# Kernel tuning notes

Hardware: AMD Instinct MI355X
Metric: run time of the kernel (lower is better)

## Reference

```python
import jax, jax.numpy as jnp
import numpy as np

N_BODIES = 3
NDOF = 3 * N_BODIES          # 9
HIDDEN = 128                 # max(16, 256//2)
EPS2 = 0.1 ** 2              # softening_eps^2
MASS_EPS = 1e-8
B = 262144
# torch.triu_indices(3, 3, 1) -> pairs (0,1),(0,2),(1,2)
PAIR_I = jnp.array([0, 0, 1])
PAIR_J = jnp.array([1, 2, 2])


def setup_inputs() -> dict:
    key = jax.random.key(0)
    ks = jax.random.split(key, 7)
    inv = lambda n: 1.0 / np.sqrt(n)  # torch Linear default init scale (uniform bound)
    return {
        "z": jax.random.normal(ks[0], (B, 2 * NDOF), jnp.float32),
        "log_m_body": jnp.zeros((N_BODIES,), jnp.float32),
        "W1": jax.random.uniform(ks[1], (HIDDEN, 1), jnp.float32, -inv(1), inv(1)),
        "b1": jax.random.uniform(ks[2], (HIDDEN,), jnp.float32, -inv(1), inv(1)),
        "W2": jax.random.uniform(ks[3], (HIDDEN, HIDDEN), jnp.float32, -inv(HIDDEN), inv(HIDDEN)),
        "b2": jax.random.uniform(ks[4], (HIDDEN,), jnp.float32, -inv(HIDDEN), inv(HIDDEN)),
        "W3": jax.random.uniform(ks[5], (1, HIDDEN), jnp.float32, -inv(HIDDEN), inv(HIDDEN)),
        "b3": jax.random.uniform(ks[6], (1,), jnp.float32, -inv(HIDDEN), inv(HIDDEN)),
    }


def _hamiltonian(z, log_m_body, W1, b1, W2, b2, W3, b3):
    q, p = z[:, :NDOF], z[:, NDOF:]
    # kinetic: T(p) = 0.5 * sum p^2 / m  (tied per-body learned mass)
    minv = 1.0 / (jnp.repeat(jnp.exp(log_m_body), 3) + MASS_EPS)  # [ndof]
    T = 0.5 * jnp.sum(p * p * minv, axis=1)                        # [B]
    # potential: softened inverse pairwise distance -> tiny MLP -> sum over pairs
    qb = q.reshape(-1, N_BODIES, 3)
    diff = qb[:, PAIR_I] - qb[:, PAIR_J]                           # [B,3,3]
    d = jnp.sqrt(jnp.sum(diff * diff, axis=-1) + EPS2)             # [B,3]
    s = (1.0 / d)[..., None]                                       # [B,3,1]
    h = jax.nn.silu(s @ W1.T + b1)                                 # [B,3,128]
    h = jax.nn.silu(h @ W2.T + b2)                                 # [B,3,128]
    v = (h @ W3.T + b3)[..., 0]                                    # [B,3]
    V = jnp.sum(v, axis=1)                                         # [B]
    return T + V


def reference(z, log_m_body, W1, b1, W2, b2, W3, b3):
    # dz/dt = J grad_z H with canonical J: dq/dt = dH/dp, dp/dt = -dH/dq
    grad = jax.grad(
        lambda zz: jnp.sum(_hamiltonian(zz, log_m_body, W1, b1, W2, b2, W3, b3))
    )(z)
    dqdt = grad[:, NDOF:]
    dpdt = -grad[:, :NDOF]
    return jnp.concatenate([dqdt, dpdt], axis=1)
```

## Files before the change

kernel.cpp:

```cpp
#include <hip/hip_runtime.h>
#include <math.h>

#define HIDDEN       128
#define TABLE_N      2048
#define SMAX         10.0f
#define E            8
#define TB_THREADS   128
#define MAIN_THREADS 256
#define EPS2         0.01f
#define MASS_EPS     1e-8f
#define W2PAD        (HIDDEN + 1)

__global__ __launch_bounds__(TB_THREADS)
void build_table_kernel(const float* __restrict__ W1,
                        const float* __restrict__ b1,
                        const float* __restrict__ W2,
                        const float* __restrict__ b2,
                        const float* __restrict__ W3,
                        const float* __restrict__ logm,
                        float* __restrict__ table)
{
    const int tid = threadIdx.x;
    const int e0  = blockIdx.x * E;
    __shared__ float w2s[HIDDEN * W2PAD];
    __shared__ float sh[HIDDEN * E];

    {
        const float4* w2v = (const float4*)W2;
        #pragma unroll
        for (int k = 0; k < (HIDDEN * HIDDEN / 4) / TB_THREADS; ++k) {
            int idx = k * TB_THREADS + tid;
            float4 v = w2v[idx];
            int fi  = idx << 2;
            int row = fi >> 7;
            int col = fi & (HIDDEN - 1);
            float* dst = &w2s[row * W2PAD + col];
            dst[0] = v.x; dst[1] = v.y; dst[2] = v.z; dst[3] = v.w;
        }
    }

    if (blockIdx.x == 0 && tid < 3)
        table[TABLE_N + tid] = 1.0f / (expf(logm[tid]) + MASS_EPS);

    const float ds  = SMAX / (float)(TABLE_N - 1);
    const float w1  = W1[tid];
    const float bb1 = b1[tid];

    float sp1[E];
    #pragma unroll
    for (int e = 0; e < E; ++e) {
        float s  = (float)(e0 + e) * ds;
        float u1 = w1 * s + bb1;
        float sg = 1.0f / (1.0f + expf(-u1));
        sh[tid * E + e] = u1 * sg;
        sp1[e] = sg * (1.0f + u1 * (1.0f - sg));
    }
    __syncthreads();

    float u2[E];
    #pragma unroll
    for (int e = 0; e < E; ++e) u2[e] = b2[tid];
    for (int j = 0; j < HIDDEN; ++j) {
        float w = w2s[tid * W2PAD + j];
        #pragma unroll
        for (int e = 0; e < E; ++e) u2[e] += w * sh[j * E + e];
    }

    const float w3 = W3[tid];
    float a[E];
    #pragma unroll
    for (int e = 0; e < E; ++e) {
        float sg = 1.0f / (1.0f + expf(-u2[e]));
        a[e] = w3 * sg * (1.0f + u2[e] * (1.0f - sg));
    }
    __syncthreads();
    #pragma unroll
    for (int e = 0; e < E; ++e) sh[tid * E + e] = a[e];
    __syncthreads();

    float gv[E];
    #pragma unroll
    for (int e = 0; e < E; ++e) gv[e] = 0.0f;
    for (int i = 0; i < HIDDEN; ++i) {
        float w = w2s[i * W2PAD + tid];
        #pragma unroll
        for (int e = 0; e < E; ++e) gv[e] += w * sh[i * E + e];
    }
    __syncthreads();

    #pragma unroll
    for (int e = 0; e < E; ++e) sh[tid * E + e] = w1 * sp1[e] * gv[e];
    __syncthreads();
    if (tid < E) {
        float g = 0.0f;
        for (int j = 0; j < HIDDEN; ++j) g += sh[j * E + tid];
        table[e0 + tid] = g;
    }
}

__global__ __launch_bounds__(MAIN_THREADS)
void hnn_grad_kernel(const float4* __restrict__ z4,
                     const float* __restrict__ table,
                     float4* __restrict__ out4)
{
    __shared__ alignas(16) float buf[MAIN_THREADS * 18];
    float4* bufv = (float4*)buf;
    const int tid = threadIdx.x;
    const long long base4 = (long long)blockIdx.x * (MAIN_THREADS * 18 / 4);

    #pragma unroll
    for (int k = 0; k < 4; ++k)
        bufv[k * MAIN_THREADS + tid] = z4[base4 + k * MAIN_THREADS + tid];
    if (tid < MAIN_THREADS / 2)
        bufv[4 * MAIN_THREADS + tid] = z4[base4 + 4 * MAIN_THREADS + tid];
    __syncthreads();

    float q[9], p[9];
    #pragma unroll
    for (int c = 0; c < 9; ++c) q[c] = buf[tid * 18 + c];
    #pragma unroll
    for (int c = 0; c < 9; ++c) p[c] = buf[tid * 18 + 9 + c];

    const float minv0 = table[TABLE_N + 0];
    const float minv1 = table[TABLE_N + 1];
    const float minv2 = table[TABLE_N + 2];

    float dq[9], dp[9];
    #pragma unroll
    for (int c = 0; c < 3; ++c) {
        dq[c]     = p[c]     * minv0;
        dq[3 + c] = p[3 + c] * minv1;
        dq[6 + c] = p[6 + c] * minv2;
    }
    #pragma unroll
    for (int c = 0; c < 9; ++c) dp[c] = 0.0f;

    const float scale = (float)(TABLE_N - 1) / SMAX;
    const int pi[3] = {0, 0, 1};
    const int pj[3] = {1, 2, 2};
    #pragma unroll
    for (int k = 0; k < 3; ++k) {
        const int i = pi[k] * 3, j = pj[k] * 3;
        float dx = q[i]     - q[j];
        float dy = q[i + 1] - q[j + 1];
        float dz = q[i + 2] - q[j + 2];
        float r2 = dx * dx + dy * dy + dz * dz + EPS2;
        float s  = 1.0f / sqrtf(r2);
        float x  = s * scale;
        int  idx = (int)x;
        idx = idx > (TABLE_N - 2) ? (TABLE_N - 2) : idx;
        float f  = x - (float)idx;
        float t0 = table[idx], t1 = table[idx + 1];
        float g  = t0 + f * (t1 - t0);
        float w = g * s * s * s;
        dp[i]     += w * dx;  dp[i + 1] += w * dy;  dp[i + 2] += w * dz;
        dp[j]     -= w * dx;  dp[j + 1] -= w * dy;  dp[j + 2] -= w * dz;
    }

    __syncthreads();
    #pragma unroll
    for (int c = 0; c < 9; ++c) buf[tid * 18 + c]     = dq[c];
    #pragma unroll
    for (int c = 0; c < 9; ++c) buf[tid * 18 + 9 + c] = dp[c];
    __syncthreads();

    #pragma unroll
    for (int k = 0; k < 4; ++k)
        out4[base4 + k * MAIN_THREADS + tid] = bufv[k * MAIN_THREADS + tid];
    if (tid < MAIN_THREADS / 2)
        out4[base4 + 4 * MAIN_THREADS + tid] = bufv[4 * MAIN_THREADS + tid];
}

extern "C" void kernel_launch(void* const* d_in, const int* in_sizes, int n_in,
                              void* d_out, int out_size, void* d_ws, size_t ws_size,
                              hipStream_t stream)
{
    const float* z   = (const float*)d_in[0];
    const float* lm  = (const float*)d_in[1];
    const float* W1  = (const float*)d_in[2];
    const float* b1  = (const float*)d_in[3];
    const float* W2  = (const float*)d_in[4];
    const float* b2  = (const float*)d_in[5];
    const float* W3  = (const float*)d_in[6];
    float* table = (float*)d_ws;

    hipLaunchKernelGGL(build_table_kernel, dim3(TABLE_N / E), dim3(TB_THREADS),
                       0, stream, W1, b1, W2, b2, W3, lm, table);

    const int B = in_sizes[0] / 18;
    hipLaunchKernelGGL(hnn_grad_kernel, dim3(B / MAIN_THREADS), dim3(MAIN_THREADS),
                       0, stream, (const float4*)z, table, (float4*)d_out);
}
```

Before: 97.45 us.

## Split table-build matvecs across two thread halves, stage table in LDS, nontemporal I/O

The table-build kernel now runs 256 threads, with each half computing partial sums over half of the hidden dimension and combining them through shared memory. Its final reduction over hidden units becomes a two-level tree. The main kernel copies the interpolation table into LDS before doing the random-index lookups, and uses nontemporal loads and stores for the streaming z and output traffic. Costs are extra shared memory, more barriers, and a per-block table copy that adds global reads.

```diff
diff --git a/kernel.cpp b/kernel.cpp
--- a/kernel.cpp
+++ b/kernel.cpp
@@ -5,11 +5,13 @@
 #define TABLE_N      2048
 #define SMAX         10.0f
 #define E            8
-#define TB_THREADS   128
+#define TB_THREADS   256
 #define MAIN_THREADS 256
 #define EPS2         0.01f
 #define MASS_EPS     1e-8f
 #define W2PAD        (HIDDEN + 1)
+
+typedef float vf4 __attribute__((ext_vector_type(4)));
 
 __global__ __launch_bounds__(TB_THREADS)
 void build_table_kernel(const float* __restrict__ W1,
@@ -20,17 +22,21 @@
                         const float* __restrict__ logm,
                         float* __restrict__ table)
 {
-    const int tid = threadIdx.x;
-    const int e0  = blockIdx.x * E;
+    const int tid  = threadIdx.x;
+    const int unit = tid & 127;
+    const int half = tid >> 7;
+    const int e0   = blockIdx.x * E;
+
     __shared__ float w2s[HIDDEN * W2PAD];
     __shared__ float sh[HIDDEN * E];
+    __shared__ float part[TB_THREADS * E];
 
     {
-        const float4* w2v = (const float4*)W2;
-        #pragma unroll
-        for (int k = 0; k < (HIDDEN * HIDDEN / 4) / TB_THREADS; ++k) {
+        const vf4* w2v = (const vf4*)W2;
+        #pragma unroll
+        for (int k = 0; k < 16; ++k) {
             int idx = k * TB_THREADS + tid;
-            float4 v = w2v[idx];
+            vf4 v = w2v[idx];
             int fi  = idx << 2;
             int row = fi >> 7;
             int col = fi & (HIDDEN - 1);
@@ -43,8 +49,8 @@
         table[TABLE_N + tid] = 1.0f / (expf(logm[tid]) + MASS_EPS);
 
     const float ds  = SMAX / (float)(TABLE_N - 1);
-    const float w1  = W1[tid];
-    const float bb1 = b1[tid];
+    const float w1  = W1[unit];
+    const float bb1 = b1[unit];
 
     float sp1[E];
     #pragma unroll
@@ -52,67 +58,99 @@
         float s  = (float)(e0 + e) * ds;
         float u1 = w1 * s + bb1;
         float sg = 1.0f / (1.0f + expf(-u1));
-        sh[tid * E + e] = u1 * sg;
+        if (half == 0) sh[unit * E + e] = u1 * sg;
         sp1[e] = sg * (1.0f + u1 * (1.0f - sg));
     }
     __syncthreads();
 
-    float u2[E];
-    #pragma unroll
-    for (int e = 0; e < E; ++e) u2[e] = b2[tid];
-    for (int j = 0; j < HIDDEN; ++j) {
-        float w = w2s[tid * W2PAD + j];
-        #pragma unroll
-        for (int e = 0; e < E; ++e) u2[e] += w * sh[j * E + e];
-    }
-
-    const float w3 = W3[tid];
-    float a[E];
-    #pragma unroll
-    for (int e = 0; e < E; ++e) {
-        float sg = 1.0f / (1.0f + expf(-u2[e]));
-        a[e] = w3 * sg * (1.0f + u2[e] * (1.0f - sg));
-    }
-    __syncthreads();
-    #pragma unroll
-    for (int e = 0; e < E; ++e) sh[tid * E + e] = a[e];
-    __syncthreads();
-
-    float gv[E];
-    #pragma unroll
-    for (int e = 0; e < E; ++e) gv[e] = 0.0f;
-    for (int i = 0; i < HIDDEN; ++i) {
-        float w = w2s[i * W2PAD + tid];
-        #pragma unroll
-        for (int e = 0; e < E; ++e) gv[e] += w * sh[i * E + e];
-    }
-    __syncthreads();
-
-    #pragma unroll
-    for (int e = 0; e < E; ++e) sh[tid * E + e] = w1 * sp1[e] * gv[e];
+    float acc[E];
+    #pragma unroll
+    for (int e = 0; e < E; ++e) acc[e] = 0.0f;
+    const int jb = half * 64;
+    for (int j = 0; j < 64; ++j) {
+        float w = w2s[unit * W2PAD + jb + j];
+        #pragma unroll
+        for (int e = 0; e < E; ++e) acc[e] += w * sh[(jb + j) * E + e];
+    }
+    #pragma unroll
+    for (int e = 0; e < E; ++e) part[tid * E + e] = acc[e];
+    __syncthreads();
+
+    if (half == 0) {
+        const float w3 = W3[unit];
+        const float bb2 = b2[unit];
+        #pragma unroll
+        for (int e = 0; e < E; ++e) {
+            float u2 = part[unit * E + e] + part[(unit + 128) * E + e] + bb2;
+            float sg = 1.0f / (1.0f + expf(-u2));
+            sh[unit * E + e] = w3 * sg * (1.0f + u2 * (1.0f - sg));
+        }
+    }
+    __syncthreads();
+
+    #pragma unroll
+    for (int e = 0; e < E; ++e) acc[e] = 0.0f;
+    const int ib = half * 64;
+    for (int i = 0; i < 64; ++i) {
+        float w = w2s[(ib + i) * W2PAD + unit];
+        #pragma unroll
+        for (int e = 0; e < E; ++e) acc[e] += w * sh[(ib + i) * E + e];
+    }
+    #pragma unroll
+    for (int e = 0; e < E; ++e) part[tid * E + e] = acc[e];
+    __syncthreads();
+
+    if (half == 0) {
+        #pragma unroll
+        for (int e = 0; e < E; ++e) {
+            float gv = part[unit * E + e] + part[(unit + 128) * E + e];
+            sh[unit * E + e] = w1 * sp1[e] * gv;
+        }
+    }
+    __syncthreads();
+
+    if (tid < 128) {
+        int e = tid & 7, chunk = tid >> 3;
+        float s = 0.0f;
+        #pragma unroll
+        for (int j = 0; j < 8; ++j) s += sh[(chunk * 8 + j) * E + e];
+        part[e * 16 + chunk] = s;
+    }
     __syncthreads();
     if (tid < E) {
         float g = 0.0f;
-        for (int j = 0; j < HIDDEN; ++j) g += sh[j * E + tid];
+        #pragma unroll
+        for (int c = 0; c < 16; ++c) g += part[tid * 16 + c];
         table[e0 + tid] = g;
     }
 }
 
 __global__ __launch_bounds__(MAIN_THREADS)
-void hnn_grad_kernel(const float4* __restrict__ z4,
+void hnn_grad_kernel(const vf4* __restrict__ z4,
                      const float* __restrict__ table,
-                     float4* __restrict__ out4)
+                     vf4* __restrict__ out4)
 {
     __shared__ alignas(16) float buf[MAIN_THREADS * 18];
-    float4* bufv = (float4*)buf;
+    __shared__ alignas(16) float tl[TABLE_N + 4];
+    vf4* bufv = (vf4*)buf;
     const int tid = threadIdx.x;
     const long long base4 = (long long)blockIdx.x * (MAIN_THREADS * 18 / 4);
 
+    {
+        const vf4* t4 = (const vf4*)table;
+        vf4* tl4 = (vf4*)tl;
+        tl4[tid]                = t4[tid];
+        tl4[MAIN_THREADS + tid] = t4[MAIN_THREADS + tid];
+        if (tid < 3) tl[TABLE_N + tid] = table[TABLE_N + tid];
+    }
+
     #pragma unroll
     for (int k = 0; k < 4; ++k)
-        bufv[k * MAIN_THREADS + tid] = z4[base4 + k * MAIN_THREADS + tid];
+        bufv[k * MAIN_THREADS + tid] =
+            __builtin_nontemporal_load(&z4[base4 + k * MAIN_THREADS + tid]);
     if (tid < MAIN_THREADS / 2)
-        bufv[4 * MAIN_THREADS + tid] = z4[base4 + 4 * MAIN_THREADS + tid];
+        bufv[4 * MAIN_THREADS + tid] =
+            __builtin_nontemporal_load(&z4[base4 + 4 * MAIN_THREADS + tid]);
     __syncthreads();
 
     float q[9], p[9];
@@ -121,9 +159,9 @@
     #pragma unroll
     for (int c = 0; c < 9; ++c) p[c] = buf[tid * 18 + 9 + c];
 
-    const float minv0 = table[TABLE_N + 0];
-    const float minv1 = table[TABLE_N + 1];
-    const float minv2 = table[TABLE_N + 2];
+    const float minv0 = tl[TABLE_N + 0];
+    const float minv1 = tl[TABLE_N + 1];
+    const float minv2 = tl[TABLE_N + 2];
 
     float dq[9], dp[9];
     #pragma unroll
@@ -150,7 +188,7 @@
         int  idx = (int)x;
         idx = idx > (TABLE_N - 2) ? (TABLE_N - 2) : idx;
         float f  = x - (float)idx;
-        float t0 = table[idx], t1 = table[idx + 1];
+        float t0 = tl[idx], t1 = tl[idx + 1];
         float g  = t0 + f * (t1 - t0);
         float w = g * s * s * s;
         dp[i]     += w * dx;  dp[i + 1] += w * dy;  dp[i + 2] += w * dz;
@@ -166,9 +204,11 @@
 
     #pragma unroll
     for (int k = 0; k < 4; ++k)
-        out4[base4 + k * MAIN_THREADS + tid] = bufv[k * MAIN_THREADS + tid];
+        __builtin_nontemporal_store(bufv[k * MAIN_THREADS + tid],
+                                    &out4[base4 + k * MAIN_THREADS + tid]);
     if (tid < MAIN_THREADS / 2)
-        out4[base4 + 4 * MAIN_THREADS + tid] = bufv[4 * MAIN_THREADS + tid];
+        __builtin_nontemporal_store(bufv[4 * MAIN_THREADS + tid],
+                                    &out4[base4 + 4 * MAIN_THREADS + tid]);
 }
 
 extern "C" void kernel_launch(void* const* d_in, const int* in_sizes, int n_in,
@@ -189,5 +229,5 @@
 
     const int B = in_sizes[0] / 18;
     hipLaunchKernelGGL(hnn_grad_kernel, dim3(B / MAIN_THREADS), dim3(MAIN_THREADS),
-                       0, stream, (const float4*)z, table, (float4*)d_out);
+                       0, stream, (const vf4*)z, table, (vf4*)d_out);
 }
```

Result: faster. 94.80 us (-2.7%).
